# Optimization experiments

Hardware: AMD Instinct MI355X
Metric: run time of the kernel (lower is better)

## Reference

```python
import jax, jax.numpy as jnp
import numpy as np
import math

EMB_DIM = 1024
N_HEADS = 16
HEAD_DIM = EMB_DIM // N_HEADS
B, T = 4, 2048


def bitlinear(x, w):
    # BitNet b1.58 absmean ternary quantization. NOTE: the source never
    # rescales the ternary weights by `scale`, so forward uses raw {-1,0,1}.
    scale = jnp.maximum(jnp.mean(jnp.abs(w)), 1e-8)
    w_ternary = jnp.clip(jnp.round(w / scale), -1.0, 1.0)
    w_q = w + jax.lax.stop_gradient(w_ternary - w)  # STE
    return x @ w_q.T


def setup_inputs() -> dict:
    key = jax.random.key(0)
    k1, k2, k3 = jax.random.split(key, 3)
    x = jax.random.normal(k1, (B, T, EMB_DIM), dtype=jnp.float32)
    w_qkv = jax.random.normal(k2, (3 * EMB_DIM, EMB_DIM), dtype=jnp.float32) * 0.02
    w_out = jax.random.normal(k3, (EMB_DIM, EMB_DIM), dtype=jnp.float32) * 0.02
    return {"x": x, "w_qkv": w_qkv, "w_out": w_out}


def reference(x, w_qkv, w_out):
    Bc, Tc, C = x.shape
    qkv = bitlinear(x, w_qkv)  # [B, T, 3C]
    q, k, v = jnp.split(qkv, 3, axis=2)

    def split_heads(t):  # [B, T, C] -> [B, H, T, D]
        return t.reshape(Bc, Tc, N_HEADS, HEAD_DIM).transpose(0, 2, 1, 3)

    q, k, v = split_heads(q), split_heads(k), split_heads(v)
    scale = math.sqrt(HEAD_DIM)
    scores = jnp.einsum("bhqd,bhkd->bhqk", q, k) / scale  # [B, H, T, T]
    causal = jnp.triu(jnp.ones((Tc, Tc), dtype=bool), k=1)
    scores = jnp.where(causal, -jnp.inf, scores)
    attn = jax.nn.softmax(scores, axis=-1)
    out = jnp.einsum("bhqk,bhkd->bhqd", attn, v)  # [B, H, T, D]
    out = out.transpose(0, 2, 1, 3).reshape(Bc, Tc, C)
    return bitlinear(out, w_out)
```

## Files before the change

kernel.cpp:

```cpp
#include <hip/hip_runtime.h>
#include <hip/hip_bf16.h>

#define EMB   1024
#define NHEAD 16
#define HDIM  64
#define BSZ   4
#define SEQ   2048
#define MROWS (BSZ*SEQ)
#define NQKV  (3*EMB)

typedef __bf16 bf16;
typedef __bf16 bf16v4 __attribute__((ext_vector_type(4)));
typedef __bf16 bf16v8 __attribute__((ext_vector_type(8)));
typedef float  f32v4  __attribute__((ext_vector_type(4)));
typedef int    i32v4  __attribute__((ext_vector_type(4)));

#define MFMA16(a,b,c)  __builtin_amdgcn_mfma_f32_16x16x32_bf16((a),(b),(c),0,0,0)
#define MFMAI8(a,b,c)  __builtin_amdgcn_mfma_i32_16x16x64_i8((a),(b),(c),0,0,0)

__device__ __forceinline__ void gload_lds16(const void* g, void* l) {
  __builtin_amdgcn_global_load_lds((const __attribute__((address_space(1))) void*)g,
                                   (__attribute__((address_space(3))) void*)l,
                                   16, 0, 0);
}


__global__ void zero2_kernel(float* p) { p[threadIdx.x] = 0.f; }

__global__ void abs_sum_kernel(const float* __restrict__ w, int n, float* out) {
  float s = 0.f;
  for (int i = blockIdx.x * blockDim.x + threadIdx.x; i < n; i += gridDim.x * blockDim.x)
    s += fabsf(w[i]);
  #pragma unroll
  for (int off = 32; off; off >>= 1) s += __shfl_down(s, off, 64);
  __shared__ float red[4];
  int lane = threadIdx.x & 63, wid = threadIdx.x >> 6;
  if (lane == 0) red[wid] = s;
  __syncthreads();
  if (threadIdx.x == 0) atomicAdd(out, red[0] + red[1] + red[2] + red[3]);
}

__global__ void ternarize_i8_kernel(const float* __restrict__ w, int n,
                                    const float* __restrict__ sum, char* __restrict__ out) {
  int i = blockIdx.x * blockDim.x + threadIdx.x;
  if (i >= n) return;
  float scale = fmaxf(*sum / (float)n, 1e-8f);
  float t = rintf(w[i] / scale);
  t = fmaxf(-1.f, fminf(1.f, t));
  out[i] = (char)(int)t;
}

__global__ void ternarize_bf16_kernel(const float* __restrict__ w, int n,
                                      const float* __restrict__ sum, bf16* __restrict__ out) {
  int i = blockIdx.x * blockDim.x + threadIdx.x;
  if (i >= n) return;
  float scale = fmaxf(*sum / (float)n, 1e-8f);
  float t = rintf(w[i] / scale);
  t = fmaxf(-1.f, fminf(1.f, t));
  out[i] = (bf16)t;
}

__global__ void quant_x_kernel(const float* __restrict__ x, char* __restrict__ p1,
                               char* __restrict__ p2, int n) {
  int i = blockIdx.x * blockDim.x + threadIdx.x;
  if (i >= n) return;
  float v = x[i];
  float q1 = fminf(fmaxf(rintf(v * 16.f), -127.f), 127.f);
  float r = v - q1 * 0.0625f;
  float q2 = fminf(fmaxf(rintf(r * 4096.f), -127.f), 127.f);
  p1[i] = (char)(int)q1;
  p2[i] = (char)(int)q2;
}


__launch_bounds__(256, 2)
__global__ void gemm_qkv_kernel(const char* __restrict__ xq1, const char* __restrict__ xq2,
                                const char* __restrict__ w8,
                                bf16* __restrict__ qh, bf16* __restrict__ ql,
                                bf16* __restrict__ kh, bf16* __restrict__ kl,
                                bf16* __restrict__ vv) {
  __shared__ __align__(16) char A1[128 * 64];
  __shared__ __align__(16) char A2[128 * 64];
  __shared__ __align__(16) char Bs[128 * 64];
  const int tid = threadIdx.x;
  const int lane = tid & 63, wid = tid >> 6;
  const int quad = lane >> 4, l16 = lane & 15;
  const int m0 = blockIdx.x * 128, n0 = blockIdx.y * 128;
  const int wm = (wid >> 1) * 64, wn = (wid & 1) * 64;
  const int asw = (l16 >> 1) & 3;
  i32v4 acc1[4][4] = {};
  i32v4 acc2[4][4] = {};

  for (int kt = 0; kt < EMB / 64; ++kt) {
    __syncthreads();
    #pragma unroll
    for (int r = 0; r < 2; ++r) {
      int li = r * 256 + tid;
      int row = li >> 2, cs = li & 3;
      int cg = cs ^ ((row >> 1) & 3);
      gload_lds16(xq1 + (size_t)(m0 + row) * EMB + kt * 64 + cg * 16, &A1[li * 16]);
      gload_lds16(xq2 + (size_t)(m0 + row) * EMB + kt * 64 + cg * 16, &A2[li * 16]);
      gload_lds16(w8  + (size_t)(n0 + row) * EMB + kt * 64 + cg * 16, &Bs[li * 16]);
    }
    __syncthreads();
    i32v4 af1[4], af2[4], bfr[4];
    #pragma unroll
    for (int i = 0; i < 4; ++i) {
      int arow = wm + i * 16 + l16;
      int off = arow * 64 + ((quad ^ asw) * 16);
      af1[i] = *(const i32v4*)&A1[off];
      af2[i] = *(const i32v4*)&A2[off];
      int brow = wn + i * 16 + l16;
      bfr[i] = *(const i32v4*)&Bs[brow * 64 + ((quad ^ asw) * 16)];
    }
    #pragma unroll
    for (int i = 0; i < 4; ++i)
      #pragma unroll
      for (int j = 0; j < 4; ++j) {
        acc1[i][j] = MFMAI8(af1[i], bfr[j], acc1[i][j]);
        acc2[i][j] = MFMAI8(af2[i], bfr[j], acc2[i][j]);
      }
  }
  const float S1 = 0.0625f, S2 = 1.f / 4096.f;
  const float QSCALE = 0.18033688011112042f;
  #pragma unroll
  for (int i = 0; i < 4; ++i)
    #pragma unroll
    for (int j = 0; j < 4; ++j)
      #pragma unroll
      for (int r = 0; r < 4; ++r) {
        int m = m0 + wm + i * 16 + quad * 4 + r;
        int n = n0 + wn + j * 16 + l16;
        float c = (float)acc1[i][j][r] * S1 + (float)acc2[i][j][r] * S2;
        int b = m >> 11, t = m & (SEQ - 1);
        int region = n >> 10, c1 = n & 1023, h = c1 >> 6, d = c1 & 63;
        size_t idx = (((size_t)(b * NHEAD + h) * SEQ + t) << 6) + d;
        if (region == 0)      { float cs = c * QSCALE; bf16 hi = (bf16)cs; qh[idx] = hi; ql[idx] = (bf16)(cs - (float)hi); }
        else if (region == 1) { bf16 hi = (bf16)c; kh[idx] = hi; kl[idx] = (bf16)(c - (float)hi); }
        else                  { vv[idx] = (bf16)c; }
      }
}


__global__ void transpose_v_kernel(const bf16* __restrict__ v, bf16* __restrict__ vt) {
  __shared__ bf16 tile[64 * 72];
  const int tid = threadIdx.x;
  const int bh = blockIdx.y, t0 = blockIdx.x * 64;
  const size_t base = (size_t)bh * SEQ * HDIM;
  #pragma unroll
  for (int r = 0; r < 2; ++r) {
    int li = r * 256 + tid;
    int row = li >> 3, col = (li & 7) * 8;
    bf16v8 val = *(const bf16v8*)(v + base + (size_t)(t0 + row) * HDIM + col);
    #pragma unroll
    for (int j = 0; j < 8; ++j) tile[(col + j) * 72 + row] = val[j];
  }
  __syncthreads();
  #pragma unroll
  for (int r = 0; r < 2; ++r) {
    int li = r * 256 + tid;
    int drow = li >> 3, tcol = (li & 7) * 8;
    bf16v8 val;
    #pragma unroll
    for (int j = 0; j < 8; ++j) val[j] = tile[drow * 72 + tcol + j];
    *(bf16v8*)(vt + base + (size_t)drow * SEQ + t0 + tcol) = val;
  }
}


__launch_bounds__(256, 2)
__global__ void attn_kernel(const bf16* __restrict__ qh, const bf16* __restrict__ ql,
                            const bf16* __restrict__ kh, const bf16* __restrict__ kl,
                            const bf16* __restrict__ vt, bf16* __restrict__ o) {
  __shared__ __align__(16) char smem[57856];
  bf16* Qh = (bf16*)smem;
  bf16* Ql = (bf16*)(smem + 16384);
  bf16* Pw = (bf16*)(smem + 49152);
  const int tid = threadIdx.x;
  const int lane = tid & 63, wid = tid >> 6;
  const int quad = lane >> 4, l16 = lane & 15;
  const int xs = l16 & 7;
  const int pair = blockIdx.x;
  const int bh = blockIdx.y;
  const size_t base = (size_t)bh * SEQ * HDIM;

  auto stage_kv = [&](char* dst, int k0) {
    #pragma unroll
    for (int r = 0; r < 2; ++r) {
      int li = r * 256 + tid;
      int srow = li >> 3, scg = (li & 7) ^ (srow & 7);
      gload_lds16(kh + base + (size_t)(k0 + srow) * HDIM + scg * 8, (bf16*)dst + (size_t)li * 8);
      gload_lds16(kl + base + (size_t)(k0 + srow) * HDIM + scg * 8, (bf16*)(dst + 8192) + (size_t)li * 8);
      gload_lds16(vt + base + (size_t)srow * SEQ + k0 + scg * 8,    (bf16*)(dst + 16384) + (size_t)li * 8);
    }
  };

  const int b = bh >> 4, h = bh & 15;
  bf16* Ps = Pw + wid * (16 * 68);

  for (int phase = 0; phase < 2; ++phase) {
    const int qt = phase ? (7 - pair) : (8 + pair);
    const int q0 = qt * 128;

    __syncthreads();
    #pragma unroll
    for (int r = 0; r < 4; ++r) {
      int li = r * 256 + tid;
      int row = li >> 3, cg = (li & 7) ^ (row & 7);
      gload_lds16(qh + base + (size_t)(q0 + row) * HDIM + cg * 8, &Qh[li * 8]);
      gload_lds16(ql + base + (size_t)(q0 + row) * HDIM + cg * 8, &Ql[li * 8]);
    }
    __syncthreads();
    bf16v8 qhf[2][2], qlf[2][2];
    #pragma unroll
    for (int sub = 0; sub < 2; ++sub)
      #pragma unroll
      for (int kk = 0; kk < 2; ++kk) {
        int off = (wid * 32 + sub * 16 + l16) * 64 + (((kk << 2) | quad) ^ xs) * 8;
        qhf[sub][kk] = *(const bf16v8*)&Qh[off];
        qlf[sub][kk] = *(const bf16v8*)&Ql[off];
      }
    __syncthreads();

    f32v4 oacc[2][4] = {};
    float lsum[2] = {0.f, 0.f};
    float mrow[2] = {-1e30f, -1e30f};

    const int qw0 = q0 + wid * 32;
    const int qrow_hi = qw0 + 31;
    const int ntiles = 2 * qt + 2;

    stage_kv(smem, 0);

    for (int ktile = 0; ktile < ntiles; ++ktile) {
      char* cb = smem + (size_t)((ktile & 1) * 24576);
      char* nb = smem + (size_t)(((ktile + 1) & 1) * 24576);
      __syncthreads();
      if (ktile + 1 < ntiles) stage_kv(nb, (ktile + 1) * 64);
      const int k0 = ktile * 64;
      if (k0 > qrow_hi) continue;

      bf16* Kh_ = (bf16*)cb;
      bf16* Kl_ = (bf16*)(cb + 8192);
      bf16* Vt_ = (bf16*)(cb + 16384);

      const bool live0 = (k0 <= qw0 + 15);

      f32v4 sacc[2][4] = {};
      #pragma unroll
      for (int kk = 0; kk < 2; ++kk) {
        const int co = (((kk << 2) | quad) ^ xs) * 8;
        bf16v8 khf[4], klf[4];
        #pragma unroll
        for (int nt = 0; nt < 4; ++nt) {
          khf[nt] = *(const bf16v8*)&Kh_[(nt * 16 + l16) * 64 + co];
          klf[nt] = *(const bf16v8*)&Kl_[(nt * 16 + l16) * 64 + co];
        }
        #pragma unroll
        for (int sub = 0; sub < 2; ++sub) {
          if (sub == 0 && !live0) continue;
          #pragma unroll
          for (int nt = 0; nt < 4; ++nt) {
            sacc[sub][nt] = MFMA16(khf[nt], qhf[sub][kk], sacc[sub][nt]);
            sacc[sub][nt] = MFMA16(klf[nt], qhf[sub][kk], sacc[sub][nt]);
            sacc[sub][nt] = MFMA16(khf[nt], qlf[sub][kk], sacc[sub][nt]);
          }
        }
      }

      #pragma unroll
      for (int sub = 0; sub < 2; ++sub) {
        if (sub == 0 && !live0) continue;
        const int dq = (qw0 + sub * 16 + l16) - k0 - quad * 4;
        #pragma unroll
        for (int nt = 0; nt < 4; ++nt)
          #pragma unroll
          for (int r = 0; r < 4; ++r)
            if (nt * 16 + r > dq) sacc[sub][nt][r] = -1e30f;

        float mA = fmaxf(fmaxf(sacc[sub][0][0], sacc[sub][0][1]),
                         fmaxf(sacc[sub][0][2], sacc[sub][0][3]));
        float mB = fmaxf(fmaxf(sacc[sub][1][0], sacc[sub][1][1]),
                         fmaxf(sacc[sub][1][2], sacc[sub][1][3]));
        float mC = fmaxf(fmaxf(sacc[sub][2][0], sacc[sub][2][1]),
                         fmaxf(sacc[sub][2][2], sacc[sub][2][3]));
        float mD = fmaxf(fmaxf(sacc[sub][3][0], sacc[sub][3][1]),
                         fmaxf(sacc[sub][3][2], sacc[sub][3][3]));
        float mx = fmaxf(fmaxf(mA, mB), fmaxf(mC, mD));
        mx = fmaxf(mx, __shfl_xor(mx, 16, 64));
        mx = fmaxf(mx, __shfl_xor(mx, 32, 64));

        const bool grow = __any(mx > mrow[sub]);
        const float mnew = grow ? fmaxf(mrow[sub], mx) : mrow[sub];

        float snt[4];
        #pragma unroll
        for (int nt = 0; nt < 4; ++nt) {
          bf16v4 t;
          float s0 = 0.f, s1 = 0.f;
          #pragma unroll
          for (int r = 0; r < 4; ++r) {
            float ev = __builtin_amdgcn_exp2f(sacc[sub][nt][r] - mnew);
            bf16 pb = (bf16)ev;
            t[r] = pb;
            if (r & 1) s1 += (float)pb; else s0 += (float)pb;
          }
          snt[nt] = s0 + s1;
          *(bf16v4*)&Ps[l16 * 68 + nt * 16 + quad * 4] = t;
        }
        float s = (snt[0] + snt[1]) + (snt[2] + snt[3]);
        s += __shfl_xor(s, 16, 64);
        s += __shfl_xor(s, 32, 64);

        if (grow) {
          const float alpha = __builtin_amdgcn_exp2f(mrow[sub] - mnew);
          mrow[sub] = mnew;
          lsum[sub] = lsum[sub] * alpha + s;
          float abp[4];
          #pragma unroll
          for (int r = 0; r < 4; ++r)
            abp[r] = __shfl(alpha, quad * 20 + r, 64);
          #pragma unroll
          for (int dt = 0; dt < 4; ++dt)
            #pragma unroll
            for (int r = 0; r < 4; ++r)
              oacc[sub][dt][r] *= abp[r];
        } else {
          lsum[sub] += s;
        }

        #pragma unroll
        for (int kk = 0; kk < 2; ++kk) {
          const int co = (((kk << 2) | quad) ^ xs) * 8;
          bf16v8 pf = *(const bf16v8*)&Ps[l16 * 68 + kk * 32 + quad * 8];
          #pragma unroll
          for (int dt = 0; dt < 4; ++dt) {
            bf16v8 vf = *(const bf16v8*)&Vt_[(dt * 16 + l16) * 64 + co];
            oacc[sub][dt] = MFMA16(pf, vf, oacc[sub][dt]);
          }
        }
      }
    }

    #pragma unroll
    for (int sub = 0; sub < 2; ++sub) {
      float lrow[4];
      #pragma unroll
      for (int r = 0; r < 4; ++r)
        lrow[r] = __shfl(lsum[sub], quad * 20 + r, 64);
      #pragma unroll
      for (int dt = 0; dt < 4; ++dt)
        #pragma unroll
        for (int r = 0; r < 4; ++r) {
          int q = q0 + wid * 32 + sub * 16 + quad * 4 + r;
          int d = dt * 16 + l16;
          float val = oacc[sub][dt][r] / lrow[r];
          o[((size_t)(b * SEQ + q)) * EMB + h * HDIM + d] = (bf16)val;
        }
    }
  }
}


__launch_bounds__(256, 2)
__global__ void gemm_out_kernel(const bf16* __restrict__ oin, const bf16* __restrict__ wt,
                                float* __restrict__ out) {
  __shared__ __align__(16) bf16 As_[128 * 64];
  __shared__ __align__(16) bf16 Bs_[128 * 64];
  const int tid = threadIdx.x;
  const int lane = tid & 63, wid = tid >> 6;
  const int quad = lane >> 4, l16 = lane & 15;
  const int m0 = blockIdx.x * 128, n0 = blockIdx.y * 128;
  const int wm = (wid >> 1) * 64, wn = (wid & 1) * 64;
  f32v4 acc[4][4] = {};

  for (int kt = 0; kt < EMB / 64; ++kt) {
    __syncthreads();
    #pragma unroll
    for (int r = 0; r < 4; ++r) {
      int li = r * 256 + tid;
      int row = li >> 3, col = (li & 7) * 8;
      gload_lds16(oin + (size_t)(m0 + row) * EMB + kt * 64 + col, &As_[li * 8]);
      gload_lds16(wt  + (size_t)(n0 + row) * EMB + kt * 64 + col, &Bs_[li * 8]);
    }
    __syncthreads();
    #pragma unroll
    for (int kk = 0; kk < 2; ++kk) {
      bf16v8 af[4], bfr[4];
      #pragma unroll
      for (int i = 0; i < 4; ++i) {
        af[i]  = *(const bf16v8*)&As_[(wm + i * 16 + l16) * 64 + kk * 32 + quad * 8];
        bfr[i] = *(const bf16v8*)&Bs_[(wn + i * 16 + l16) * 64 + kk * 32 + quad * 8];
      }
      #pragma unroll
      for (int i = 0; i < 4; ++i)
        #pragma unroll
        for (int j = 0; j < 4; ++j)
          acc[i][j] = MFMA16(af[i], bfr[j], acc[i][j]);
    }
  }
  #pragma unroll
  for (int i = 0; i < 4; ++i)
    #pragma unroll
    for (int j = 0; j < 4; ++j)
      #pragma unroll
      for (int r = 0; r < 4; ++r) {
        int m = m0 + wm + i * 16 + quad * 4 + r;
        int n = n0 + wn + j * 16 + l16;
        out[(size_t)m * EMB + n] = acc[i][j][r];
      }
}


extern "C" void kernel_launch(void* const* d_in, const int* in_sizes, int n_in,
                              void* d_out, int out_size, void* d_ws, size_t ws_size,
                              hipStream_t stream) {
  const float* x     = (const float*)d_in[0];
  const float* w_qkv = (const float*)d_in[1];
  const float* w_out = (const float*)d_in[2];
  float* out = (float*)d_out;
  char* ws = (char*)d_ws;

  const size_t SZ  = (size_t)MROWS * EMB * sizeof(bf16);
  const size_t SZ8 = (size_t)MROWS * EMB;
  size_t off = 0;
  float* sums = (float*)ws;            off = 256;
  char*  wq8  = (char*)(ws + off);     off += (size_t)NQKV * EMB;
  bf16*  wo_t = (bf16*)(ws + off);     off += (size_t)EMB * EMB * sizeof(bf16);
  char*  xq1  = (char*)(ws + off);     off += SZ8;
  char*  xq2  = (char*)(ws + off);     off += SZ8;
  bf16*  qh   = (bf16*)(ws + off);     off += SZ;
  bf16*  ql   = (bf16*)(ws + off);     off += SZ;
  bf16*  kh   = (bf16*)(ws + off);     off += SZ;
  bf16*  kl   = (bf16*)(ws + off);     off += SZ;
  bf16*  vv   = (bf16*)(ws + off);     off += SZ;
  bf16*  vt   = (bf16*)xq1;
  bf16*  ob   = vv;
  (void)in_sizes; (void)n_in; (void)out_size; (void)ws_size;

  zero2_kernel<<<1, 2, 0, stream>>>(sums);
  abs_sum_kernel<<<256, 256, 0, stream>>>(w_qkv, NQKV * EMB, &sums[0]);
  abs_sum_kernel<<<256, 256, 0, stream>>>(w_out, EMB * EMB, &sums[1]);
  ternarize_i8_kernel<<<(NQKV * EMB) / 256, 256, 0, stream>>>(w_qkv, NQKV * EMB, &sums[0], wq8);
  ternarize_bf16_kernel<<<(EMB * EMB) / 256, 256, 0, stream>>>(w_out, EMB * EMB, &sums[1], wo_t);
  quant_x_kernel<<<(MROWS * EMB) / 256, 256, 0, stream>>>(x, xq1, xq2, MROWS * EMB);
  gemm_qkv_kernel<<<dim3(MROWS / 128, NQKV / 128), 256, 0, stream>>>(xq1, xq2, wq8, qh, ql, kh, kl, vv);
  transpose_v_kernel<<<dim3(SEQ / 64, BSZ * NHEAD), 256, 0, stream>>>(vv, vt);
  attn_kernel<<<dim3(8, BSZ * NHEAD), 256, 0, stream>>>(qh, ql, kh, kl, vt, ob);
  gemm_out_kernel<<<dim3(MROWS / 128, EMB / 128), 256, 0, stream>>>(ob, wo_t, out);
}
```

Baseline: 366.1 us.

## Keep softmax probabilities in registers and permute V loads to match MFMA layout

Removes the per-wave LDS staging buffer for the P matrix. The probabilities are packed straight from the QK accumulator registers into PV MFMA operands, and the V reads are reordered into two 4-element halves so their k-ordering matches the register layout. This frees LDS, allowing launch bounds of 3 blocks per CU, and shares each V fragment across both sub-tiles. It also drops the live0 skip, so fully masked sub-tiles now get computed, and the higher occupancy target may cause register spills.

```diff
diff --git a/kernel.cpp b/kernel.cpp
--- a/kernel.cpp
+++ b/kernel.cpp
@@ -168,14 +168,13 @@
 }
 
 
-__launch_bounds__(256, 2)
+__launch_bounds__(256, 3)
 __global__ void attn_kernel(const bf16* __restrict__ qh, const bf16* __restrict__ ql,
                             const bf16* __restrict__ kh, const bf16* __restrict__ kl,
                             const bf16* __restrict__ vt, bf16* __restrict__ o) {
-  __shared__ __align__(16) char smem[57856];
+  __shared__ __align__(16) char smem[49152];
   bf16* Qh = (bf16*)smem;
   bf16* Ql = (bf16*)(smem + 16384);
-  bf16* Pw = (bf16*)(smem + 49152);
   const int tid = threadIdx.x;
   const int lane = tid & 63, wid = tid >> 6;
   const int quad = lane >> 4, l16 = lane & 15;
@@ -196,7 +195,7 @@
   };
 
   const int b = bh >> 4, h = bh & 15;
-  bf16* Ps = Pw + wid * (16 * 68);
+  union pb8 { bf16v8 v; int w[4]; };
 
   for (int phase = 0; phase < 2; ++phase) {
     const int qt = phase ? (7 - pair) : (8 + pair);
@@ -244,8 +243,6 @@
       bf16* Kl_ = (bf16*)(cb + 8192);
       bf16* Vt_ = (bf16*)(cb + 16384);
 
-      const bool live0 = (k0 <= qw0 + 15);
-
       f32v4 sacc[2][4] = {};
       #pragma unroll
       for (int kk = 0; kk < 2; ++kk) {
@@ -257,20 +254,18 @@
           klf[nt] = *(const bf16v8*)&Kl_[(nt * 16 + l16) * 64 + co];
         }
         #pragma unroll
-        for (int sub = 0; sub < 2; ++sub) {
-          if (sub == 0 && !live0) continue;
+        for (int sub = 0; sub < 2; ++sub)
           #pragma unroll
           for (int nt = 0; nt < 4; ++nt) {
             sacc[sub][nt] = MFMA16(khf[nt], qhf[sub][kk], sacc[sub][nt]);
             sacc[sub][nt] = MFMA16(klf[nt], qhf[sub][kk], sacc[sub][nt]);
             sacc[sub][nt] = MFMA16(khf[nt], qlf[sub][kk], sacc[sub][nt]);
           }
-        }
-      }
-
+      }
+
+      pb8 pa[2][2];
       #pragma unroll
       for (int sub = 0; sub < 2; ++sub) {
-        if (sub == 0 && !live0) continue;
         const int dq = (qw0 + sub * 16 + l16) - k0 - quad * 4;
         #pragma unroll
         for (int nt = 0; nt < 4; ++nt)
@@ -297,16 +292,18 @@
         #pragma unroll
         for (int nt = 0; nt < 4; ++nt) {
           bf16v4 t;
-          float s0 = 0.f, s1 = 0.f;
+          float ss0 = 0.f, ss1 = 0.f;
           #pragma unroll
           for (int r = 0; r < 4; ++r) {
             float ev = __builtin_amdgcn_exp2f(sacc[sub][nt][r] - mnew);
             bf16 pb = (bf16)ev;
             t[r] = pb;
-            if (r & 1) s1 += (float)pb; else s0 += (float)pb;
+            if (r & 1) ss1 += (float)pb; else ss0 += (float)pb;
           }
-          snt[nt] = s0 + s1;
-          *(bf16v4*)&Ps[l16 * 68 + nt * 16 + quad * 4] = t;
+          snt[nt] = ss0 + ss1;
+          union { bf16v4 v; int w[2]; } u; u.v = t;
+          pa[sub][nt >> 1].w[(nt & 1) * 2]     = u.w[0];
+          pa[sub][nt >> 1].w[(nt & 1) * 2 + 1] = u.w[1];
         }
         float s = (snt[0] + snt[1]) + (snt[2] + snt[3]);
         s += __shfl_xor(s, 16, 64);
@@ -328,16 +325,21 @@
         } else {
           lsum[sub] += s;
         }
-
-        #pragma unroll
-        for (int kk = 0; kk < 2; ++kk) {
-          const int co = (((kk << 2) | quad) ^ xs) * 8;
-          bf16v8 pf = *(const bf16v8*)&Ps[l16 * 68 + kk * 32 + quad * 8];
-          #pragma unroll
-          for (int dt = 0; dt < 4; ++dt) {
-            bf16v8 vf = *(const bf16v8*)&Vt_[(dt * 16 + l16) * 64 + co];
-            oacc[sub][dt] = MFMA16(pf, vf, oacc[sub][dt]);
-          }
+      }
+
+      #pragma unroll
+      for (int kk = 0; kk < 2; ++kk) {
+        const int o_lo = (((kk * 4 +     (quad >> 1)) ^ xs) * 8) + (quad & 1) * 4;
+        const int o_hi = (((kk * 4 + 2 + (quad >> 1)) ^ xs) * 8) + (quad & 1) * 4;
+        #pragma unroll
+        for (int dt = 0; dt < 4; ++dt) {
+          const bf16* rowp = &Vt_[(dt * 16 + l16) * 64];
+          union { bf16v8 v; bf16v4 h[2]; } vu;
+          vu.h[0] = *(const bf16v4*)&rowp[o_lo];
+          vu.h[1] = *(const bf16v4*)&rowp[o_hi];
+          #pragma unroll
+          for (int sub = 0; sub < 2; ++sub)
+            oacc[sub][dt] = MFMA16(pa[sub][kk].v, vu.v, oacc[sub][dt]);
         }
       }
     }
```

New measurement: 381.7 us. 4.3% more time.
